# Performance work log

Measured on AMD Instinct MI355X. Metric: run time of the kernel, lower is better.

The kernel has to match this reference:

```python
import jax, jax.numpy as jnp
import numpy as np

N_IN, N_OT, E, D = 100000, 50000, 1000000, 64


def setup_inputs() -> dict:
    key = jax.random.key(0)
    ks = jax.random.split(key, 14)
    s = 1.0 / np.sqrt(D)
    return {
        "input": jax.random.normal(ks[0], (N_IN, D), jnp.float32),
        "other": jax.random.normal(ks[1], (N_OT, D), jnp.float32),
        "rj": jax.random.randint(ks[2], (E,), 0, N_IN),
        "lj": jax.random.randint(ks[3], (E,), 0, N_OT),
        "weights": jax.random.normal(ks[4], (E, 1), jnp.float32),
        # self.input: Linear(D, D)
        "Wi": jax.random.normal(ks[5], (D, D), jnp.float32) * s,
        "bi": jax.random.normal(ks[6], (D,), jnp.float32) * s,
        # self.other: Linear(D, D, bias=False)
        "Wo": jax.random.normal(ks[7], (D, D), jnp.float32) * s,
        # self.edges: Linear(1, D, bias=False) stored as [1, D]
        "We": jax.random.normal(ks[8], (1, D), jnp.float32),
        # self.final[1]: Linear(D, D)
        "Wf": jax.random.normal(ks[9], (D, D), jnp.float32) * s,
        "bf": jax.random.normal(ks[10], (D,), jnp.float32) * s,
        # self.output: Linear(2D, D)  (mlp strips trailing activation)
        "Wout": jax.random.normal(ks[11], (2 * D, D), jnp.float32) * (1.0 / np.sqrt(2 * D)),
        "bout": jax.random.normal(ks[12], (D,), jnp.float32) * (1.0 / np.sqrt(2 * D)),
    }


def reference(input, other, rj, lj, weights, Wi, bi, Wo, We, Wf, bf, Wout, bout):
    rhs = input @ Wi + bi                       # [N_IN, D]
    lhs = other @ Wo                            # [N_OT, D]
    message = rhs[rj] + lhs[lj] + weights @ We  # [E, D] gather + edge embed
    msg = jax.nn.leaky_relu(message, 0.01) @ Wf + bf
    out = jax.ops.segment_sum(msg, rj, num_segments=input.shape[0])  # [N_IN, D]
    return jnp.concatenate([out, input], axis=-1) @ Wout + bout
```

## Files before the change

kernel.cpp:

```cpp
#include <hip/hip_runtime.h>
#include <hip/hip_bf16.h>


typedef short short8 __attribute__((ext_vector_type(8)));
typedef float f32x4  __attribute__((ext_vector_type(4)));

static __device__ __forceinline__ float bf2f(unsigned u) {
    return __uint_as_float(u << 16);
}
static __device__ __forceinline__ unsigned f2bf(float f) {
    unsigned u = __float_as_uint(f);
    return (u + 0x7fffu + ((u >> 16) & 1u)) >> 16;
}

__global__ void prep_weights(const float* __restrict__ Wi, const float* __restrict__ Wo,
                             const float* __restrict__ Wf, const float* __restrict__ bf,
                             const float* __restrict__ Wout,
                             unsigned short* __restrict__ WiT,
                             unsigned short* __restrict__ WoT,
                             unsigned short* __restrict__ WcatT,
                             float* __restrict__ bcomb) {
    int id = blockIdx.x * blockDim.x + threadIdx.x;
    if (id < 8192) {
        int n = id >> 7, k = id & 127;
        float v;
        if (k < 64) {
            v = 0.f;
#pragma unroll 8
            for (int j = 0; j < 64; ++j) v = fmaf(Wf[k * 64 + j], Wout[j * 64 + n], v);
        } else {
            v = Wout[k * 64 + n];
        }
        WcatT[id] = (unsigned short)f2bf(v);
    } else if (id < 8256) {
        int n = id - 8192;
        float v = 0.f;
#pragma unroll 8
        for (int j = 0; j < 64; ++j) v = fmaf(bf[j], Wout[j * 64 + n], v);
        bcomb[n] = v;
    } else if (id < 12352) {
        int t = id - 8256, n = t >> 6, k = t & 63;
        WiT[t] = (unsigned short)f2bf(Wi[k * 64 + n]);
    } else if (id < 16448) {
        int t = id - 12352, n = t >> 6, k = t & 63;
        WoT[t] = (unsigned short)f2bf(Wo[k * 64 + n]);
    }
}

__global__ void mfma_rowgemm(const float* __restrict__ X,
                             const unsigned short* __restrict__ WT,
                             const float* __restrict__ b,
                             unsigned short* __restrict__ Y,
                             unsigned short* __restrict__ Xb, int N) {
    const int lane = threadIdx.x & 63;
    const int wave = (blockIdx.x * blockDim.x + threadIdx.x) >> 6;
    const long long base = (long long)wave * 16;
    if (base >= N) return;
    const int r15 = lane & 15, hi = lane >> 4;
    long long arow = base + r15;
    if (arow >= N) arow = N - 1;

    short8 afr[2];
#pragma unroll
    for (int s = 0; s < 2; ++s) {
        const int kb = s * 32 + hi * 8;
        const float* px = X + arow * 64 + kb;
        float4 x0 = *(const float4*)px;
        float4 x1 = *(const float4*)(px + 4);
        short8 a;
        a[0] = (short)f2bf(x0.x); a[1] = (short)f2bf(x0.y);
        a[2] = (short)f2bf(x0.z); a[3] = (short)f2bf(x0.w);
        a[4] = (short)f2bf(x1.x); a[5] = (short)f2bf(x1.y);
        a[6] = (short)f2bf(x1.z); a[7] = (short)f2bf(x1.w);
        afr[s] = a;
        if (Xb) *(short8*)(Xb + arow * 64 + kb) = a;
    }
    const f32x4 z = {0.f, 0.f, 0.f, 0.f};
    f32x4 acc[4] = {z, z, z, z};
#pragma unroll
    for (int t = 0; t < 4; ++t)
#pragma unroll
        for (int s = 0; s < 2; ++s) {
            short8 bb = *(const short8*)(WT + (t * 16 + r15) * 64 + s * 32 + hi * 8);
            acc[t] = __builtin_amdgcn_mfma_f32_16x16x32_bf16(afr[s], bb, acc[t], 0, 0, 0);
        }
#pragma unroll
    for (int t = 0; t < 4; ++t) {
        const int col = t * 16 + r15;
        const float bv = b ? b[col] : 0.f;
#pragma unroll
        for (int j = 0; j < 4; ++j) {
            long long row = base + hi * 4 + j;
            if (row < N) Y[row * 64 + col] = (unsigned short)f2bf(acc[t][j] + bv);
        }
    }
}

__global__ void hist_kernel(const int* __restrict__ rj, int* __restrict__ deg, int E) {
    int i = blockIdx.x * blockDim.x + threadIdx.x, st = gridDim.x * blockDim.x;
    for (; i < E; i += st) atomicAdd(&deg[rj[i]], 1);
}

__global__ void scan1_kernel(const int* __restrict__ deg, int* __restrict__ rowoff,
                             int* __restrict__ blksum, int N) {
    __shared__ int s[1024];
    const int tid = threadIdx.x;
    const int i = blockIdx.x * 1024 + tid;
    int v = (i < N) ? deg[i] : 0;
    s[tid] = v;
    __syncthreads();
    for (int off = 1; off < 1024; off <<= 1) {
        int t = (tid >= off) ? s[tid - off] : 0;
        __syncthreads();
        s[tid] += t;
        __syncthreads();
    }
    if (i < N) rowoff[i] = s[tid] - v;
    if (tid == 1023) blksum[blockIdx.x] = s[1023];
}

__global__ void scan2_kernel(int* __restrict__ blksum, int nb) {
    __shared__ int s[1024];
    const int tid = threadIdx.x;
    int v = (tid < nb) ? blksum[tid] : 0;
    s[tid] = v;
    __syncthreads();
    for (int off = 1; off < 1024; off <<= 1) {
        int t = (tid >= off) ? s[tid - off] : 0;
        __syncthreads();
        s[tid] += t;
        __syncthreads();
    }
    if (tid < nb) blksum[tid] = s[tid] - v;
}

__global__ void scan3_kernel(int* __restrict__ rowoff, const int* __restrict__ blksum,
                             int* __restrict__ cursor, int N, int E) {
    int i = blockIdx.x * blockDim.x + threadIdx.x, st = gridDim.x * blockDim.x;
    for (; i < N; i += st) {
        int v = rowoff[i] + blksum[i >> 10];
        rowoff[i] = v;
        cursor[i] = v;
    }
    if (blockIdx.x == 0 && threadIdx.x == 0) rowoff[N] = E;
}

__global__ void scatter_kernel(const int* __restrict__ rj, const int* __restrict__ lj,
                               const float* __restrict__ wts, int* __restrict__ cursor,
                               int2* __restrict__ pay, int E) {
    const int tid0 = blockIdx.x * blockDim.x + threadIdx.x;
    const int st = gridDim.x * blockDim.x;
    for (int s = 0; s <= 6; ++s) {
        for (int i = tid0; i < E; i += st) {
            int r = rj[i];
            if ((r >> 14) == s) {
                int pos = atomicAdd(&cursor[r], 1);
                pay[pos] = make_int2(lj[i], __float_as_int(wts[i]));
            }
        }
    }
}

__global__ void reduce_kernel(const unsigned short* __restrict__ rhs,
                              const unsigned short* __restrict__ lhs,
                              const int2* __restrict__ pay,
                              const float* __restrict__ We,
                              const int* __restrict__ rowoff,
                              unsigned short* __restrict__ S, int N) {
    const int lane = threadIdx.x & 63;
    const int wid  = threadIdx.x >> 6;
    const int wpb  = blockDim.x >> 6;
    const float wev = We[lane];
    const int w0 = blockIdx.x * wpb + wid;
    const int wtot = gridDim.x * wpb;
    for (int row = w0; row < N; row += wtot) {
        const int beg = rowoff[row], end = rowoff[row + 1];
        const float rv = bf2f(rhs[(size_t)row * 64 + lane]);
        float s = 0.f;
        int idx = beg;
        for (; idx + 8 <= end; idx += 8) {
            int2 p[8];
#pragma unroll
            for (int j = 0; j < 8; ++j) p[j] = pay[idx + j];
            float a[8];
#pragma unroll
            for (int j = 0; j < 8; ++j) a[j] = bf2f(lhs[(size_t)p[j].x * 64 + lane]);
#pragma unroll
            for (int j = 0; j < 8; ++j) {
                float m = rv + a[j] + __int_as_float(p[j].y) * wev;
                s += (m >= 0.f) ? m : 0.01f * m;
            }
        }
        if (idx + 4 <= end) {
            int2 p[4];
#pragma unroll
            for (int j = 0; j < 4; ++j) p[j] = pay[idx + j];
#pragma unroll
            for (int j = 0; j < 4; ++j) {
                float m = rv + bf2f(lhs[(size_t)p[j].x * 64 + lane])
                          + __int_as_float(p[j].y) * wev;
                s += (m >= 0.f) ? m : 0.01f * m;
            }
            idx += 4;
        }
        for (; idx < end; ++idx) {
            int2 p = pay[idx];
            float m = rv + bf2f(lhs[(size_t)p.x * 64 + lane])
                      + __int_as_float(p.y) * wev;
            s += (m >= 0.f) ? m : 0.01f * m;
        }
        S[(size_t)row * 64 + lane] = (unsigned short)f2bf(s);
    }
}

__global__ void final_mfma(const unsigned short* __restrict__ S,
                           const unsigned short* __restrict__ Xb,
                           const unsigned short* __restrict__ WcatT,
                           const float* __restrict__ bcomb,
                           const float* __restrict__ bout,
                           const int* __restrict__ deg,
                           float* __restrict__ out, int N) {
    const int lane = threadIdx.x & 63;
    const int wave = (blockIdx.x * blockDim.x + threadIdx.x) >> 6;
    const long long base = (long long)wave * 16;
    if (base >= N) return;
    const int r15 = lane & 15, hi = lane >> 4;
    long long arow = base + r15;
    if (arow >= N) arow = N - 1;

    short8 afr[4];
#pragma unroll
    for (int s = 0; s < 2; ++s)
        afr[s] = *(const short8*)(S + arow * 64 + s * 32 + hi * 8);
#pragma unroll
    for (int s = 0; s < 2; ++s)
        afr[2 + s] = *(const short8*)(Xb + arow * 64 + s * 32 + hi * 8);

    const f32x4 z = {0.f, 0.f, 0.f, 0.f};
    f32x4 acc[4] = {z, z, z, z};
#pragma unroll
    for (int t = 0; t < 4; ++t)
#pragma unroll
        for (int s = 0; s < 4; ++s) {
            short8 bb = *(const short8*)(WcatT + (t * 16 + r15) * 128 + s * 32 + hi * 8);
            acc[t] = __builtin_amdgcn_mfma_f32_16x16x32_bf16(afr[s], bb, acc[t], 0, 0, 0);
        }

    float dj[4];
#pragma unroll
    for (int j = 0; j < 4; ++j) {
        long long rr = base + hi * 4 + j;
        dj[j] = (rr < N) ? (float)deg[rr] : 0.f;
    }
#pragma unroll
    for (int t = 0; t < 4; ++t) {
        const int col = t * 16 + r15;
        const float bc = bcomb[col];
        const float bo = bout[col];
#pragma unroll
        for (int j = 0; j < 4; ++j) {
            long long rr = base + hi * 4 + j;
            if (rr < N) out[rr * 64 + col] = fmaf(dj[j], bc, acc[t][j] + bo);
        }
    }
}

extern "C" void kernel_launch(void* const* d_in, const int* in_sizes, int n_in,
                              void* d_out, int out_size, void* d_ws, size_t ws_size,
                              hipStream_t stream) {
    const float* input = (const float*)d_in[0];
    const float* other = (const float*)d_in[1];
    const int*   rj    = (const int*)d_in[2];
    const int*   lj    = (const int*)d_in[3];
    const float* wts   = (const float*)d_in[4];
    const float* Wi    = (const float*)d_in[5];
    const float* bi    = (const float*)d_in[6];
    const float* Wo    = (const float*)d_in[7];
    const float* We    = (const float*)d_in[8];
    const float* Wf    = (const float*)d_in[9];
    const float* bf    = (const float*)d_in[10];
    const float* Wout  = (const float*)d_in[11];
    const float* bout  = (const float*)d_in[12];
    float* out = (float*)d_out;

    const int N_IN = in_sizes[0] / 64;
    const int N_OT = in_sizes[1] / 64;
    const int E    = in_sizes[2];
    const int nb1  = (N_IN + 1023) / 1024;

    char* ws = (char*)d_ws;
    int2* pay = (int2*)ws;                        ws += (size_t)E * sizeof(int2);
    unsigned short* WiT   = (unsigned short*)ws;  ws += 4096 * 2;
    unsigned short* WoT   = (unsigned short*)ws;  ws += 4096 * 2;
    unsigned short* WcatT = (unsigned short*)ws;  ws += 8192 * 2;
    float* bcomb = (float*)ws;                    ws += 64 * sizeof(float);
    int* deg     = (int*)ws;                      ws += (size_t)N_IN * sizeof(int);
    int* rowoff  = (int*)ws;                      ws += ((size_t)N_IN + 2) * sizeof(int);
    int* cursor  = (int*)ws;                      ws += (size_t)N_IN * sizeof(int);
    int* blksum  = (int*)ws;                      ws += 1024 * sizeof(int);
    unsigned short* rhs = (unsigned short*)ws;    ws += (size_t)N_IN * 64 * 2;
    unsigned short* lhs = (unsigned short*)ws;    ws += (size_t)N_OT * 64 * 2;
    unsigned short* S   = (unsigned short*)ws;    ws += (size_t)N_IN * 64 * 2;
    unsigned short* Xb  = (unsigned short*)ws;    ws += (size_t)N_IN * 64 * 2;

    hipMemsetAsync(deg, 0, (size_t)N_IN * sizeof(int), stream);

    prep_weights<<<65, 256, 0, stream>>>(Wi, Wo, Wf, bf, Wout, WiT, WoT, WcatT, bcomb);

    const int gbA = (N_IN + 63) / 64;
    const int gbB = (N_OT + 63) / 64;
    mfma_rowgemm<<<gbA, 256, 0, stream>>>(input, WiT, bi, rhs, Xb, N_IN);
    mfma_rowgemm<<<gbB, 256, 0, stream>>>(other, WoT, nullptr, lhs, nullptr, N_OT);

    hist_kernel<<<1024, 256, 0, stream>>>(rj, deg, E);
    scan1_kernel<<<nb1, 1024, 0, stream>>>(deg, rowoff, blksum, N_IN);
    scan2_kernel<<<1, 1024, 0, stream>>>(blksum, nb1);
    scan3_kernel<<<256, 256, 0, stream>>>(rowoff, blksum, cursor, N_IN, E);
    scatter_kernel<<<1024, 256, 0, stream>>>(rj, lj, wts, cursor, pay, E);

    reduce_kernel<<<2048, 256, 0, stream>>>(rhs, lhs, pay, We, rowoff, S, N_IN);
    final_mfma<<<gbA, 256, 0, stream>>>(S, Xb, WcatT, bcomb, bout, deg, out, N_IN);
}
```

Before: 300.0 us.

## Pack edge payload into 32 bits and run scatter as parallel bucket groups

The histogram kernel now also writes a packed 32-bit payload per edge, holding the 16-bit lj index and the edge weight rounded to bf16. This halves payload traffic in both scatter and reduce. The scatter kernel no longer makes seven sequential passes over all edges; the grid is split into 8 block groups, each handling one bucket of destination rows. Rounding the weight to bf16 lowers accuracy, and the 16-bit index packing only works while N_OT stays under 65536.

```diff
diff --git a/kernel.cpp b/kernel.cpp
--- a/kernel.cpp
+++ b/kernel.cpp
@@ -96,9 +96,15 @@
     }
 }
 
-__global__ void hist_kernel(const int* __restrict__ rj, int* __restrict__ deg, int E) {
+__global__ void pack_hist_kernel(const int* __restrict__ rj, const int* __restrict__ lj,
+                                 const float* __restrict__ wts,
+                                 unsigned* __restrict__ pk, int* __restrict__ deg,
+                                 int E) {
     int i = blockIdx.x * blockDim.x + threadIdx.x, st = gridDim.x * blockDim.x;
-    for (; i < E; i += st) atomicAdd(&deg[rj[i]], 1);
+    for (; i < E; i += st) {
+        atomicAdd(&deg[rj[i]], 1);
+        pk[i] = (unsigned)lj[i] | (f2bf(wts[i]) << 16);
+    }
 }
 
 __global__ void scan1_kernel(const int* __restrict__ deg, int* __restrict__ rowoff,
@@ -145,25 +151,24 @@
     if (blockIdx.x == 0 && threadIdx.x == 0) rowoff[N] = E;
 }
 
-__global__ void scatter_kernel(const int* __restrict__ rj, const int* __restrict__ lj,
-                               const float* __restrict__ wts, int* __restrict__ cursor,
-                               int2* __restrict__ pay, int E) {
-    const int tid0 = blockIdx.x * blockDim.x + threadIdx.x;
-    const int st = gridDim.x * blockDim.x;
-    for (int s = 0; s <= 6; ++s) {
-        for (int i = tid0; i < E; i += st) {
-            int r = rj[i];
-            if ((r >> 14) == s) {
-                int pos = atomicAdd(&cursor[r], 1);
-                pay[pos] = make_int2(lj[i], __float_as_int(wts[i]));
-            }
+__global__ void scatter_kernel(const int* __restrict__ rj, const unsigned* __restrict__ pk,
+                               int* __restrict__ cursor, unsigned* __restrict__ pay,
+                               int E) {
+    const int g    = blockIdx.x & 7;
+    const int gblk = blockIdx.x >> 3;
+    const int st   = (gridDim.x >> 3) * blockDim.x;
+    for (int i = gblk * blockDim.x + threadIdx.x; i < E; i += st) {
+        int r = rj[i];
+        if (((r >> 13) & 7) == g) {
+            int pos = atomicAdd(&cursor[r], 1);
+            pay[pos] = pk[i];
         }
     }
 }
 
 __global__ void reduce_kernel(const unsigned short* __restrict__ rhs,
                               const unsigned short* __restrict__ lhs,
-                              const int2* __restrict__ pay,
+                              const unsigned* __restrict__ pay,
                               const float* __restrict__ We,
                               const int* __restrict__ rowoff,
                               unsigned short* __restrict__ S, int N) {
@@ -179,34 +184,35 @@
         float s = 0.f;
         int idx = beg;
         for (; idx + 8 <= end; idx += 8) {
-            int2 p[8];
+            unsigned p[8];
 #pragma unroll
             for (int j = 0; j < 8; ++j) p[j] = pay[idx + j];
             float a[8];
 #pragma unroll
-            for (int j = 0; j < 8; ++j) a[j] = bf2f(lhs[(size_t)p[j].x * 64 + lane]);
+            for (int j = 0; j < 8; ++j)
+                a[j] = bf2f(lhs[(size_t)(p[j] & 0xffffu) * 64 + lane]);
 #pragma unroll
             for (int j = 0; j < 8; ++j) {
-                float m = rv + a[j] + __int_as_float(p[j].y) * wev;
+                float m = rv + a[j] + bf2f(p[j] >> 16) * wev;
                 s += (m >= 0.f) ? m : 0.01f * m;
             }
         }
         if (idx + 4 <= end) {
-            int2 p[4];
+            unsigned p[4];
 #pragma unroll
             for (int j = 0; j < 4; ++j) p[j] = pay[idx + j];
 #pragma unroll
             for (int j = 0; j < 4; ++j) {
-                float m = rv + bf2f(lhs[(size_t)p[j].x * 64 + lane])
-                          + __int_as_float(p[j].y) * wev;
+                float m = rv + bf2f(lhs[(size_t)(p[j] & 0xffffu) * 64 + lane])
+                          + bf2f(p[j] >> 16) * wev;
                 s += (m >= 0.f) ? m : 0.01f * m;
             }
             idx += 4;
         }
         for (; idx < end; ++idx) {
-            int2 p = pay[idx];
-            float m = rv + bf2f(lhs[(size_t)p.x * 64 + lane])
-                      + __int_as_float(p.y) * wev;
+            unsigned p = pay[idx];
+            float m = rv + bf2f(lhs[(size_t)(p & 0xffffu) * 64 + lane])
+                      + bf2f(p >> 16) * wev;
             s += (m >= 0.f) ? m : 0.01f * m;
         }
         S[(size_t)row * 64 + lane] = (unsigned short)f2bf(s);
@@ -289,7 +295,8 @@
     const int nb1  = (N_IN + 1023) / 1024;
 
     char* ws = (char*)d_ws;
-    int2* pay = (int2*)ws;                        ws += (size_t)E * sizeof(int2);
+    unsigned* pay = (unsigned*)ws;                ws += (size_t)E * sizeof(unsigned);
+    unsigned* pk  = (unsigned*)ws;                ws += (size_t)E * sizeof(unsigned);
     unsigned short* WiT   = (unsigned short*)ws;  ws += 4096 * 2;
     unsigned short* WoT   = (unsigned short*)ws;  ws += 4096 * 2;
     unsigned short* WcatT = (unsigned short*)ws;  ws += 8192 * 2;
@@ -312,11 +319,11 @@
     mfma_rowgemm<<<gbA, 256, 0, stream>>>(input, WiT, bi, rhs, Xb, N_IN);
     mfma_rowgemm<<<gbB, 256, 0, stream>>>(other, WoT, nullptr, lhs, nullptr, N_OT);
 
-    hist_kernel<<<1024, 256, 0, stream>>>(rj, deg, E);
+    pack_hist_kernel<<<1024, 256, 0, stream>>>(rj, lj, wts, pk, deg, E);
     scan1_kernel<<<nb1, 1024, 0, stream>>>(deg, rowoff, blksum, N_IN);
     scan2_kernel<<<1, 1024, 0, stream>>>(blksum, nb1);
     scan3_kernel<<<256, 256, 0, stream>>>(rowoff, blksum, cursor, N_IN, E);
-    scatter_kernel<<<1024, 256, 0, stream>>>(rj, lj, wts, cursor, pay, E);
+    scatter_kernel<<<1024, 256, 0, stream>>>(rj, pk, cursor, pay, E);
 
     reduce_kernel<<<2048, 256, 0, stream>>>(rhs, lhs, pay, We, rowoff, S, N_IN);
     final_mfma<<<gbA, 256, 0, stream>>>(S, Xb, WcatT, bcomb, bout, deg, out, N_IN);
```

New measurement: 293.8 us. 1.02x faster.

## Replace per-row CSR scatter with bucketed partition and LDS-atomic reduction

Applied to the files above, without the earlier changes.

Swaps the full counting-sort scatter (seven passes over the edges with per-row global atomics) for a coarse partition into 256-row buckets, using block-local LDS histograms and one global atomic per bucket per block. A new reduce kernel keeps a 256x64 float accumulator in LDS for each bucket and adds edge contributions with LDS atomics. It also fuses the histogram into weight prep, merges both projection GEMMs into one launch, folds scan2/scan3 into one kernel, and drops the Xb bf16 copy by converting input inside the final GEMM. Edge weights are now stored as bf16 and lj is packed into 16 bits, which only works while N_OT is below 65536; LDS atomic contention and uneven bucket sizes add risk.

```diff
diff --git a/kernel.cpp b/kernel.cpp
--- a/kernel.cpp
+++ b/kernel.cpp
@@ -1,6 +1,8 @@
 #include <hip/hip_runtime.h>
 #include <hip/hip_bf16.h>
 
+
+#define NBUCK_CAP 512
 
 typedef short short8 __attribute__((ext_vector_type(8)));
 typedef float f32x4  __attribute__((ext_vector_type(4)));
@@ -13,14 +15,15 @@
     return (u + 0x7fffu + ((u >> 16) & 1u)) >> 16;
 }
 
-__global__ void prep_weights(const float* __restrict__ Wi, const float* __restrict__ Wo,
-                             const float* __restrict__ Wf, const float* __restrict__ bf,
-                             const float* __restrict__ Wout,
-                             unsigned short* __restrict__ WiT,
-                             unsigned short* __restrict__ WoT,
-                             unsigned short* __restrict__ WcatT,
-                             float* __restrict__ bcomb) {
-    int id = blockIdx.x * blockDim.x + threadIdx.x;
+__global__ void prologue(const float* __restrict__ Wi, const float* __restrict__ Wo,
+                         const float* __restrict__ Wf, const float* __restrict__ bf,
+                         const float* __restrict__ Wout,
+                         unsigned short* __restrict__ WiT,
+                         unsigned short* __restrict__ WoT,
+                         unsigned short* __restrict__ WcatT,
+                         float* __restrict__ bcomb,
+                         const int* __restrict__ rj, int* __restrict__ deg, int E) {
+    const int id = blockIdx.x * blockDim.x + threadIdx.x;
     if (id < 8192) {
         int n = id >> 7, k = id & 127;
         float v;
@@ -45,15 +48,17 @@
         int t = id - 12352, n = t >> 6, k = t & 63;
         WoT[t] = (unsigned short)f2bf(Wo[k * 64 + n]);
     }
-}
-
-__global__ void mfma_rowgemm(const float* __restrict__ X,
-                             const unsigned short* __restrict__ WT,
-                             const float* __restrict__ b,
-                             unsigned short* __restrict__ Y,
-                             unsigned short* __restrict__ Xb, int N) {
+    const int st = gridDim.x * blockDim.x;
+    for (int i = id; i < E; i += st) atomicAdd(&deg[rj[i]], 1);
+}
+
+static __device__ __forceinline__ void proj_core(const float* __restrict__ X,
+                                                 const unsigned short* __restrict__ WT,
+                                                 const float* __restrict__ b,
+                                                 unsigned short* __restrict__ Y,
+                                                 int N, int bid) {
     const int lane = threadIdx.x & 63;
-    const int wave = (blockIdx.x * blockDim.x + threadIdx.x) >> 6;
+    const int wave = (bid * (int)blockDim.x + (int)threadIdx.x) >> 6;
     const long long base = (long long)wave * 16;
     if (base >= N) return;
     const int r15 = lane & 15, hi = lane >> 4;
@@ -73,7 +78,6 @@
         a[4] = (short)f2bf(x1.x); a[5] = (short)f2bf(x1.y);
         a[6] = (short)f2bf(x1.z); a[7] = (short)f2bf(x1.w);
         afr[s] = a;
-        if (Xb) *(short8*)(Xb + arow * 64 + kb) = a;
     }
     const f32x4 z = {0.f, 0.f, 0.f, 0.f};
     f32x4 acc[4] = {z, z, z, z};
@@ -96,9 +100,15 @@
     }
 }
 
-__global__ void hist_kernel(const int* __restrict__ rj, int* __restrict__ deg, int E) {
-    int i = blockIdx.x * blockDim.x + threadIdx.x, st = gridDim.x * blockDim.x;
-    for (; i < E; i += st) atomicAdd(&deg[rj[i]], 1);
+__global__ void mfma_proj(const float* __restrict__ input, const float* __restrict__ other,
+                          const unsigned short* __restrict__ WiT,
+                          const unsigned short* __restrict__ WoT,
+                          const float* __restrict__ bi,
+                          unsigned short* __restrict__ rhs,
+                          unsigned short* __restrict__ lhs,
+                          int N_IN, int N_OT, int gbA) {
+    if ((int)blockIdx.x < gbA) proj_core(input, WiT, bi, rhs, N_IN, blockIdx.x);
+    else                       proj_core(other, WoT, nullptr, lhs, N_OT, blockIdx.x - gbA);
 }
 
 __global__ void scan1_kernel(const int* __restrict__ deg, int* __restrict__ rowoff,
@@ -119,8 +129,11 @@
     if (tid == 1023) blksum[blockIdx.x] = s[1023];
 }
 
-__global__ void scan2_kernel(int* __restrict__ blksum, int nb) {
+__global__ void scan2fin(int* __restrict__ blksum, int* __restrict__ rowoff,
+                         int* __restrict__ bucketCursor, int nb, int nbuck,
+                         int N, int E) {
     __shared__ int s[1024];
+    __shared__ int ex[1024];
     const int tid = threadIdx.x;
     int v = (tid < nb) ? blksum[tid] : 0;
     s[tid] = v;
@@ -131,90 +144,87 @@
         s[tid] += t;
         __syncthreads();
     }
-    if (tid < nb) blksum[tid] = s[tid] - v;
-}
-
-__global__ void scan3_kernel(int* __restrict__ rowoff, const int* __restrict__ blksum,
-                             int* __restrict__ cursor, int N, int E) {
-    int i = blockIdx.x * blockDim.x + threadIdx.x, st = gridDim.x * blockDim.x;
-    for (; i < N; i += st) {
-        int v = rowoff[i] + blksum[i >> 10];
-        rowoff[i] = v;
-        cursor[i] = v;
-    }
-    if (blockIdx.x == 0 && threadIdx.x == 0) rowoff[N] = E;
-}
-
-__global__ void scatter_kernel(const int* __restrict__ rj, const int* __restrict__ lj,
-                               const float* __restrict__ wts, int* __restrict__ cursor,
-                               int2* __restrict__ pay, int E) {
-    const int tid0 = blockIdx.x * blockDim.x + threadIdx.x;
-    const int st = gridDim.x * blockDim.x;
-    for (int s = 0; s <= 6; ++s) {
-        for (int i = tid0; i < E; i += st) {
-            int r = rj[i];
-            if ((r >> 14) == s) {
-                int pos = atomicAdd(&cursor[r], 1);
-                pay[pos] = make_int2(lj[i], __float_as_int(wts[i]));
-            }
-        }
-    }
-}
-
-__global__ void reduce_kernel(const unsigned short* __restrict__ rhs,
-                              const unsigned short* __restrict__ lhs,
-                              const int2* __restrict__ pay,
-                              const float* __restrict__ We,
-                              const int* __restrict__ rowoff,
-                              unsigned short* __restrict__ S, int N) {
+    ex[tid] = s[tid] - v;
+    __syncthreads();
+    for (int i = tid; i < N; i += 1024) rowoff[i] += ex[i >> 10];
+    if (tid == 0) rowoff[N] = E;
+    __syncthreads();
+    for (int b = tid; b < nbuck; b += 1024) bucketCursor[b] = rowoff[b << 8];
+}
+
+__global__ void partitionA(const int* __restrict__ rj, const int* __restrict__ lj,
+                           const float* __restrict__ wts,
+                           int* __restrict__ bucketCursor,
+                           unsigned long long* __restrict__ bkt, int E, int nblk) {
+    __shared__ int cnt[NBUCK_CAP];
+    const int chunk = (E + nblk - 1) / nblk;
+    const int c0 = blockIdx.x * chunk;
+    const int c1 = (c0 + chunk < E) ? c0 + chunk : E;
+    for (int b = threadIdx.x; b < NBUCK_CAP; b += blockDim.x) cnt[b] = 0;
+    __syncthreads();
+    for (int i = c0 + threadIdx.x; i < c1; i += blockDim.x)
+        atomicAdd(&cnt[rj[i] >> 8], 1);
+    __syncthreads();
+    for (int b = threadIdx.x; b < NBUCK_CAP; b += blockDim.x) {
+        int c = cnt[b];
+        cnt[b] = c ? atomicAdd(&bucketCursor[b], c) : 0;
+    }
+    __syncthreads();
+    for (int i = c0 + threadIdx.x; i < c1; i += blockDim.x) {
+        int r = rj[i];
+        int pos = atomicAdd(&cnt[r >> 8], 1);
+        unsigned pk = (unsigned)lj[i] | (f2bf(wts[i]) << 16);
+        bkt[pos] = ((unsigned long long)r << 32) | pk;
+    }
+}
+
+__global__ __launch_bounds__(1024) void bucket_reduce(
+        const unsigned short* __restrict__ rhs, const unsigned short* __restrict__ lhs,
+        const unsigned long long* __restrict__ bkt, const float* __restrict__ We,
+        const int* __restrict__ rowoff, unsigned short* __restrict__ S, int N) {
+    __shared__ float Sl[256 * 64];
+    const int rbase = blockIdx.x << 8;
+    const int rend  = (rbase + 256 < N) ? rbase + 256 : N;
+    for (int i = threadIdx.x; i < 256 * 64; i += blockDim.x) Sl[i] = 0.f;
     const int lane = threadIdx.x & 63;
-    const int wid  = threadIdx.x >> 6;
-    const int wpb  = blockDim.x >> 6;
+    const int wv   = threadIdx.x >> 6;
     const float wev = We[lane];
-    const int w0 = blockIdx.x * wpb + wid;
-    const int wtot = gridDim.x * wpb;
-    for (int row = w0; row < N; row += wtot) {
-        const int beg = rowoff[row], end = rowoff[row + 1];
-        const float rv = bf2f(rhs[(size_t)row * 64 + lane]);
-        float s = 0.f;
-        int idx = beg;
-        for (; idx + 8 <= end; idx += 8) {
-            int2 p[8];
-#pragma unroll
-            for (int j = 0; j < 8; ++j) p[j] = pay[idx + j];
-            float a[8];
-#pragma unroll
-            for (int j = 0; j < 8; ++j) a[j] = bf2f(lhs[(size_t)p[j].x * 64 + lane]);
-#pragma unroll
-            for (int j = 0; j < 8; ++j) {
-                float m = rv + a[j] + __int_as_float(p[j].y) * wev;
-                s += (m >= 0.f) ? m : 0.01f * m;
-            }
-        }
-        if (idx + 4 <= end) {
-            int2 p[4];
-#pragma unroll
-            for (int j = 0; j < 4; ++j) p[j] = pay[idx + j];
-#pragma unroll
-            for (int j = 0; j < 4; ++j) {
-                float m = rv + bf2f(lhs[(size_t)p[j].x * 64 + lane])
-                          + __int_as_float(p[j].y) * wev;
-                s += (m >= 0.f) ? m : 0.01f * m;
-            }
-            idx += 4;
-        }
-        for (; idx < end; ++idx) {
-            int2 p = pay[idx];
-            float m = rv + bf2f(lhs[(size_t)p.x * 64 + lane])
-                      + __int_as_float(p.y) * wev;
-            s += (m >= 0.f) ? m : 0.01f * m;
-        }
-        S[(size_t)row * 64 + lane] = (unsigned short)f2bf(s);
-    }
+    const int beg = rowoff[rbase], end = rowoff[rend];
+    __syncthreads();
+    int e = beg + wv;
+    for (; e + 7 * 16 < end; e += 128) {
+        unsigned long long p[8];
+#pragma unroll
+        for (int j = 0; j < 8; ++j) p[j] = bkt[e + j * 16];
+        float av[8], rv[8];
+#pragma unroll
+        for (int j = 0; j < 8; ++j) {
+            av[j] = bf2f(lhs[(size_t)(p[j] & 0xffffu) * 64 + lane]);
+            rv[j] = bf2f(rhs[(size_t)(p[j] >> 32) * 64 + lane]);
+        }
+#pragma unroll
+        for (int j = 0; j < 8; ++j) {
+            float m = rv[j] + av[j] + bf2f((unsigned)(p[j] >> 16) & 0xffffu) * wev;
+            float val = (m >= 0.f) ? m : 0.01f * m;
+            atomicAdd(&Sl[(((int)(p[j] >> 32) - rbase) << 6) + lane], val);
+        }
+    }
+    for (; e < end; e += 16) {
+        unsigned long long p = bkt[e];
+        float m = bf2f(rhs[(size_t)(p >> 32) * 64 + lane])
+                + bf2f(lhs[(size_t)(p & 0xffffu) * 64 + lane])
+                + bf2f((unsigned)(p >> 16) & 0xffffu) * wev;
+        float val = (m >= 0.f) ? m : 0.01f * m;
+        atomicAdd(&Sl[(((int)(p >> 32) - rbase) << 6) + lane], val);
+    }
+    __syncthreads();
+    const int nel = (rend - rbase) << 6;
+    for (int i = threadIdx.x; i < nel; i += blockDim.x)
+        S[(size_t)rbase * 64 + i] = (unsigned short)f2bf(Sl[i]);
 }
 
 __global__ void final_mfma(const unsigned short* __restrict__ S,
-                           const unsigned short* __restrict__ Xb,
+                           const float* __restrict__ input,
                            const unsigned short* __restrict__ WcatT,
                            const float* __restrict__ bcomb,
                            const float* __restrict__ bout,
@@ -233,8 +243,17 @@
     for (int s = 0; s < 2; ++s)
         afr[s] = *(const short8*)(S + arow * 64 + s * 32 + hi * 8);
 #pragma unroll
-    for (int s = 0; s < 2; ++s)
-        afr[2 + s] = *(const short8*)(Xb + arow * 64 + s * 32 + hi * 8);
+    for (int s = 0; s < 2; ++s) {
+        const float* px = input + arow * 64 + s * 32 + hi * 8;
+        float4 x0 = *(const float4*)px;
+        float4 x1 = *(const float4*)(px + 4);
+        short8 a;
+        a[0] = (short)f2bf(x0.x); a[1] = (short)f2bf(x0.y);
+        a[2] = (short)f2bf(x0.z); a[3] = (short)f2bf(x0.w);
+        a[4] = (short)f2bf(x1.x); a[5] = (short)f2bf(x1.y);
+        a[6] = (short)f2bf(x1.z); a[7] = (short)f2bf(x1.w);
+        afr[2 + s] = a;
+    }
 
     const f32x4 z = {0.f, 0.f, 0.f, 0.f};
     f32x4 acc[4] = {z, z, z, z};
@@ -286,38 +305,39 @@
     const int N_IN = in_sizes[0] / 64;
     const int N_OT = in_sizes[1] / 64;
     const int E    = in_sizes[2];
-    const int nb1  = (N_IN + 1023) / 1024;
+    const int nb1   = (N_IN + 1023) / 1024;
+    const int nbuck = (N_IN + 255) / 256;
 
     char* ws = (char*)d_ws;
-    int2* pay = (int2*)ws;                        ws += (size_t)E * sizeof(int2);
+    unsigned long long* bkt = (unsigned long long*)ws; ws += (size_t)E * 8;
     unsigned short* WiT   = (unsigned short*)ws;  ws += 4096 * 2;
     unsigned short* WoT   = (unsigned short*)ws;  ws += 4096 * 2;
     unsigned short* WcatT = (unsigned short*)ws;  ws += 8192 * 2;
     float* bcomb = (float*)ws;                    ws += 64 * sizeof(float);
     int* deg     = (int*)ws;                      ws += (size_t)N_IN * sizeof(int);
     int* rowoff  = (int*)ws;                      ws += ((size_t)N_IN + 2) * sizeof(int);
-    int* cursor  = (int*)ws;                      ws += (size_t)N_IN * sizeof(int);
+    int* bucketCursor = (int*)ws;                 ws += NBUCK_CAP * sizeof(int);
     int* blksum  = (int*)ws;                      ws += 1024 * sizeof(int);
     unsigned short* rhs = (unsigned short*)ws;    ws += (size_t)N_IN * 64 * 2;
     unsigned short* lhs = (unsigned short*)ws;    ws += (size_t)N_OT * 64 * 2;
     unsigned short* S   = (unsigned short*)ws;    ws += (size_t)N_IN * 64 * 2;
-    unsigned short* Xb  = (unsigned short*)ws;    ws += (size_t)N_IN * 64 * 2;
 
     hipMemsetAsync(deg, 0, (size_t)N_IN * sizeof(int), stream);
 
-    prep_weights<<<65, 256, 0, stream>>>(Wi, Wo, Wf, bf, Wout, WiT, WoT, WcatT, bcomb);
+    prologue<<<1024, 256, 0, stream>>>(Wi, Wo, Wf, bf, Wout, WiT, WoT, WcatT, bcomb,
+                                       rj, deg, E);
 
     const int gbA = (N_IN + 63) / 64;
     const int gbB = (N_OT + 63) / 64;
-    mfma_rowgemm<<<gbA, 256, 0, stream>>>(input, WiT, bi, rhs, Xb, N_IN);
-    mfma_rowgemm<<<gbB, 256, 0, stream>>>(other, WoT, nullptr, lhs, nullptr, N_OT);
-
-    hist_kernel<<<1024, 256, 0, stream>>>(rj, deg, E);
+    mfma_proj<<<gbA + gbB, 256, 0, stream>>>(input, other, WiT, WoT, bi,
+                                             rhs, lhs, N_IN, N_OT, gbA);
+
     scan1_kernel<<<nb1, 1024, 0, stream>>>(deg, rowoff, blksum, N_IN);
-    scan2_kernel<<<1, 1024, 0, stream>>>(blksum, nb1);
-    scan3_kernel<<<256, 256, 0, stream>>>(rowoff, blksum, cursor, N_IN, E);
-    scatter_kernel<<<1024, 256, 0, stream>>>(rj, lj, wts, cursor, pay, E);
-
-    reduce_kernel<<<2048, 256, 0, stream>>>(rhs, lhs, pay, We, rowoff, S, N_IN);
-    final_mfma<<<gbA, 256, 0, stream>>>(S, Xb, WcatT, bcomb, bout, deg, out, N_IN);
-}
+    scan2fin<<<1, 1024, 0, stream>>>(blksum, rowoff, bucketCursor, nb1, nbuck, N_IN, E);
+
+    partitionA<<<128, 256, 0, stream>>>(rj, lj, wts, bucketCursor, bkt, E, 128);
+
+    bucket_reduce<<<nbuck, 1024, 0, stream>>>(rhs, lhs, bkt, We, rowoff, S, N_IN);
+
+    final_mfma<<<gbA, 256, 0, stream>>>(S, input, WcatT, bcomb, bout, deg, out, N_IN);
+}
```

Result: slower. 674.4 us (+124.8%).
